# Kernel tuning notes

Measured on AMD Instinct MI355X. Metric: run time of the kernel, lower is better.

The kernel has to match this reference:

```python
import jax, jax.numpy as jnp
import numpy as np

NUM_HEADS = 8      # SD1.x UNet cross-attn heads at 64x64 block
NUM_PROMPTS = 4    # batch = 2*NUM_PROMPTS (uncond + cond CFG halves)


def setup_inputs() -> dict:
    key = jax.random.key(0)
    ks = jax.random.split(key, 8)
    B, T, C = 2 * NUM_PROMPTS, 4096, 320   # spatial tokens, inner dim
    S, D = 77, 768                          # CLIP text seq len / width
    return {
        "hidden_states": jax.random.normal(ks[0], (B, T, C), jnp.float32),
        "encoder_hidden_states": jax.random.normal(ks[1], (B, S, D), jnp.float32),
        "mapper": jax.random.uniform(ks[2], (NUM_PROMPTS - 1, S, S), jnp.float32),
        "Wq": jax.random.normal(ks[3], (C, C), jnp.float32) * 0.02,
        "Wk": jax.random.normal(ks[4], (D, C), jnp.float32) * 0.02,
        "Wv": jax.random.normal(ks[5], (D, C), jnp.float32) * 0.02,
        "Wo": jax.random.normal(ks[6], (C, C), jnp.float32) * 0.02,
        "bo": jnp.zeros((C,), jnp.float32),
    }


def reference(hidden_states, encoder_hidden_states, mapper, Wq, Wk, Wv, Wo, bo):
    B, T, C = hidden_states.shape
    S = encoder_hidden_states.shape[1]
    H = NUM_HEADS
    d = C // H
    scale = 1.0 / jnp.sqrt(jnp.asarray(d, hidden_states.dtype))

    # projections + head split (diffusers head_to_batch_dim layout)
    q = (hidden_states @ Wq).reshape(B, T, H, d)
    k = (encoder_hidden_states @ Wk).reshape(B, S, H, d)
    v = (encoder_hidden_states @ Wv).reshape(B, S, H, d)

    # full attention probabilities must be materialized for the P2P swap
    scores = jnp.einsum('bthd,bshd->bhts', q, k) * scale
    probs = jax.nn.softmax(scores, axis=-1)  # [B, H, T, S]

    # conditional (CFG) half: [P, H, T, S]; swap via mapper einsum (cross-attn,
    # cur_step < num_steps_cross branch of swap_attention_probs)
    half = B // 2
    uncond = probs[:half]
    cond = probs[half:]
    attn_base = cond[0]                                   # [H, T, S]
    replaced = jnp.einsum('htm,pme->phte', attn_base, mapper)  # [P-1, H, T, S]
    cond = jnp.concatenate([attn_base[None], replaced], axis=0)
    probs = jnp.concatenate([uncond, cond], axis=0)

    # value matmul + merge heads (batch_to_head_dim) + output projection
    out = jnp.einsum('bhts,bshd->bthd', probs, v).reshape(B, T, C)
    return out @ Wo + bo
```

## Files before the change

### kernel.cpp

```cpp
#include <hip/hip_runtime.h>
#include <hip/hip_bf16.h>

typedef unsigned short ushort;
typedef __attribute__((ext_vector_type(8))) short bf16x8;
typedef __attribute__((ext_vector_type(8))) unsigned short ushort8;
typedef __attribute__((ext_vector_type(4))) float f32x4;
typedef __attribute__((ext_vector_type(4))) float float4v;

__device__ __forceinline__ ushort f2bf(float f) {
    union { float f; unsigned u; } v; v.f = f;
    unsigned r = v.u + 0x7FFFu + ((v.u >> 16) & 1u);
    return (ushort)(r >> 16);
}
__device__ __forceinline__ float bf2f(ushort u) {
    union { unsigned u; float f; } v; v.u = ((unsigned)u) << 16;
    return v.f;
}

__global__ __launch_bounds__(256) void transpose_all(
    const float* __restrict__ Wq, const float* __restrict__ Wk,
    const float* __restrict__ Wv, const float* __restrict__ Wo,
    ushort* __restrict__ Wq_t, ushort* __restrict__ Wk_t,
    ushort* __restrict__ Wv_t, ushort* __restrict__ Wo_t)
{
    __shared__ ushort t[32][33];
    int b = blockIdx.x;
    const float* src; ushort* dst; int K; int tb;
    if (b < 100)      { src = Wq; dst = Wq_t; K = 320; tb = b; }
    else if (b < 340) { src = Wk; dst = Wk_t; K = 768; tb = b - 100; }
    else if (b < 580) { src = Wv; dst = Wv_t; K = 768; tb = b - 340; }
    else              { src = Wo; dst = Wo_t; K = 320; tb = b - 580; }
    int tc = tb % 10, tr = tb / 10;
    int tx = threadIdx.x & 31, ty = threadIdx.x >> 5;
    #pragma unroll
    for (int p = 0; p < 4; ++p) {
        int k = tr * 32 + ty + p * 8, n = tc * 32 + tx;
        t[ty + p * 8][tx] = f2bf(src[(size_t)k * 320 + n]);
    }
    __syncthreads();
    #pragma unroll
    for (int p = 0; p < 4; ++p) {
        int n = tc * 32 + ty + p * 8, k = tr * 32 + tx;
        dst[(size_t)n * K + k] = t[tx][ty + p * 8];
    }
}

__global__ __launch_bounds__(256) void gemm_qkv(
    const float* __restrict__ A, const ushort* __restrict__ Wq_t,
    const float* __restrict__ E, const ushort* __restrict__ Wk_t,
    const ushort* __restrict__ Wv_t,
    ushort* __restrict__ Qb, float* __restrict__ part)
{
    __shared__ ushort A_lds[2][64 * 40];
    __shared__ ushort B_lds[2][320 * 40];
    const int tid = threadIdx.x;
    const int w = tid >> 6, l = tid & 63;
    const int c15 = l & 15, khi = (l >> 4) * 8;
    const int r = tid >> 2, p = (tid & 3) * 8;
    const int rbase = (l >> 4) * 4;
    f32x4 acc[4][5] = {};
    const int bid = blockIdx.x;

    if (bid < 160) {
        const int mtile = bid % 10, mat = (bid / 10) & 1, ks = bid / 20;
        const int m0 = mtile * 64, kk0 = ks * 96;
        const ushort* Bt = mat ? Wv_t : Wk_t;
        const int m = m0 + r;
        const bool live = (m < 616);
        const float* Abase = E + (size_t)(live ? m : 0) * 768 + p;
        float4v a0 = {0,0,0,0}, a1 = {0,0,0,0};
        ushort8 breg[5];
        if (live) { a0 = *(const float4v*)(Abase + kk0); a1 = *(const float4v*)(Abase + kk0 + 4); }
        #pragma unroll
        for (int i = 0; i < 5; ++i) {
            int idx = tid + i * 256; int n = idx >> 2, q = (idx & 3) * 8;
            breg[i] = *(const ushort8*)(Bt + (size_t)n * 768 + kk0 + q);
        }
        {
            ushort* d = &A_lds[0][r * 40 + p];
            d[0]=f2bf(a0.x); d[1]=f2bf(a0.y); d[2]=f2bf(a0.z); d[3]=f2bf(a0.w);
            d[4]=f2bf(a1.x); d[5]=f2bf(a1.y); d[6]=f2bf(a1.z); d[7]=f2bf(a1.w);
            #pragma unroll
            for (int i = 0; i < 5; ++i) {
                int idx = tid + i * 256; int n = idx >> 2, q = (idx & 3) * 8;
                *(ushort8*)&B_lds[0][n * 40 + q] = breg[i];
            }
        }
        __syncthreads();
        for (int k = 0; k < 3; ++k) {
            const int cur = k & 1;
            if (k < 2) {
                int kk = kk0 + (k + 1) * 32;
                if (live) { a0 = *(const float4v*)(Abase + kk); a1 = *(const float4v*)(Abase + kk + 4); }
                #pragma unroll
                for (int i = 0; i < 5; ++i) {
                    int idx = tid + i * 256; int n = idx >> 2, q = (idx & 3) * 8;
                    breg[i] = *(const ushort8*)(Bt + (size_t)n * 768 + kk + q);
                }
            }
            bf16x8 a[4];
            #pragma unroll
            for (int mf = 0; mf < 4; ++mf)
                a[mf] = *(const bf16x8*)&A_lds[cur][(mf * 16 + c15) * 40 + khi];
            #pragma unroll
            for (int f = 0; f < 5; ++f) {
                bf16x8 b = *(const bf16x8*)&B_lds[cur][(w * 80 + f * 16 + c15) * 40 + khi];
                #pragma unroll
                for (int mf = 0; mf < 4; ++mf)
                    acc[mf][f] = __builtin_amdgcn_mfma_f32_16x16x32_bf16(a[mf], b, acc[mf][f], 0, 0, 0);
            }
            if (k < 2) {
                const int nxt = cur ^ 1;
                ushort* d = &A_lds[nxt][r * 40 + p];
                d[0]=f2bf(a0.x); d[1]=f2bf(a0.y); d[2]=f2bf(a0.z); d[3]=f2bf(a0.w);
                d[4]=f2bf(a1.x); d[5]=f2bf(a1.y); d[6]=f2bf(a1.z); d[7]=f2bf(a1.w);
                #pragma unroll
                for (int i = 0; i < 5; ++i) {
                    int idx = tid + i * 256; int n = idx >> 2, q = (idx & 3) * 8;
                    *(ushort8*)&B_lds[nxt][n * 40 + q] = breg[i];
                }
                __syncthreads();
            }
        }
        float* dst = part + (size_t)(mat * 8 + ks) * 640 * 320;
        #pragma unroll
        for (int mf = 0; mf < 4; ++mf)
            #pragma unroll
            for (int f = 0; f < 5; ++f) {
                int col = w * 80 + f * 16 + c15;
                #pragma unroll
                for (int rr = 0; rr < 4; ++rr)
                    dst[(size_t)(m0 + mf * 16 + rbase + rr) * 320 + col] = acc[mf][f][rr];
            }
    } else {
        const int m0 = (bid - 160) * 64;
        const float* Abase = A + (size_t)(m0 + r) * 320 + p;
        float4v a0, a1; ushort8 breg[5];
        a0 = *(const float4v*)(Abase + 0);
        a1 = *(const float4v*)(Abase + 4);
        #pragma unroll
        for (int i = 0; i < 5; ++i) {
            int idx = tid + i * 256; int n = idx >> 2, q = (idx & 3) * 8;
            breg[i] = *(const ushort8*)(Wq_t + (size_t)n * 320 + q);
        }
        {
            ushort* d = &A_lds[0][r * 40 + p];
            d[0]=f2bf(a0.x); d[1]=f2bf(a0.y); d[2]=f2bf(a0.z); d[3]=f2bf(a0.w);
            d[4]=f2bf(a1.x); d[5]=f2bf(a1.y); d[6]=f2bf(a1.z); d[7]=f2bf(a1.w);
            #pragma unroll
            for (int i = 0; i < 5; ++i) {
                int idx = tid + i * 256; int n = idx >> 2, q = (idx & 3) * 8;
                *(ushort8*)&B_lds[0][n * 40 + q] = breg[i];
            }
        }
        __syncthreads();
        for (int k = 0; k < 10; ++k) {
            const int cur = k & 1;
            if (k < 9) {
                int kk = (k + 1) * 32;
                a0 = *(const float4v*)(Abase + kk);
                a1 = *(const float4v*)(Abase + kk + 4);
                #pragma unroll
                for (int i = 0; i < 5; ++i) {
                    int idx = tid + i * 256; int n = idx >> 2, q = (idx & 3) * 8;
                    breg[i] = *(const ushort8*)(Wq_t + (size_t)n * 320 + kk + q);
                }
            }
            bf16x8 a[4];
            #pragma unroll
            for (int mf = 0; mf < 4; ++mf)
                a[mf] = *(const bf16x8*)&A_lds[cur][(mf * 16 + c15) * 40 + khi];
            #pragma unroll
            for (int f = 0; f < 5; ++f) {
                bf16x8 b = *(const bf16x8*)&B_lds[cur][(w * 80 + f * 16 + c15) * 40 + khi];
                #pragma unroll
                for (int mf = 0; mf < 4; ++mf)
                    acc[mf][f] = __builtin_amdgcn_mfma_f32_16x16x32_bf16(a[mf], b, acc[mf][f], 0, 0, 0);
            }
            if (k < 9) {
                const int nxt = cur ^ 1;
                ushort* d = &A_lds[nxt][r * 40 + p];
                d[0]=f2bf(a0.x); d[1]=f2bf(a0.y); d[2]=f2bf(a0.z); d[3]=f2bf(a0.w);
                d[4]=f2bf(a1.x); d[5]=f2bf(a1.y); d[6]=f2bf(a1.z); d[7]=f2bf(a1.w);
                #pragma unroll
                for (int i = 0; i < 5; ++i) {
                    int idx = tid + i * 256; int n = idx >> 2, q = (idx & 3) * 8;
                    *(ushort8*)&B_lds[nxt][n * 40 + q] = breg[i];
                }
                __syncthreads();
            }
        }
        #pragma unroll
        for (int mf = 0; mf < 4; ++mf)
            #pragma unroll
            for (int f = 0; f < 5; ++f) {
                int col = w * 80 + f * 16 + c15;
                #pragma unroll
                for (int rr = 0; rr < 4; ++rr)
                    Qb[(size_t)(m0 + mf * 16 + rbase + rr) * 320 + col] = f2bf(acc[mf][f][rr]);
            }
    }
}

__global__ __launch_bounds__(256) void kv_reduce(
    const float* __restrict__ part, ushort* __restrict__ Kb, ushort* __restrict__ VVt)
{
    int idx = blockIdx.x * 256 + threadIdx.x;
    int mat = blockIdx.y;
    if (mat == 1) {
        if (idx < 8 * 320 * 3) {
            int b = idx / 960, r2 = idx - b * 960, c = r2 / 3, j = r2 - c * 3;
            VVt[((size_t)b * 320 + c) * 80 + 77 + j] = 0;
        }
    }
    if (idx >= 616 * 320) return;
    int row = idx / 320, col = idx - row * 320;
    float s = 0.f;
    #pragma unroll
    for (int ks = 0; ks < 8; ++ks)
        s += part[((size_t)(mat * 8 + ks) * 640 + row) * 320 + col];
    ushort b = f2bf(s);
    if (mat == 0) {
        Kb[(size_t)row * 320 + col] = b;
    } else {
        int bt = row / 77, ss = row - bt * 77;
        VVt[((size_t)bt * 320 + col) * 80 + ss] = b;
    }
}

__global__ void vprime_k(const float* __restrict__ mapper, const ushort* __restrict__ VVt,
                         ushort* __restrict__ VPt)
{
    int pm = blockIdx.x;
    int p = pm / 77, m = pm - p * 77;
    __shared__ float mp[77];
    int tid = threadIdx.x;
    if (tid < 77) mp[tid] = mapper[(size_t)pm * 77 + tid];
    __syncthreads();
    const ushort* vrow = VVt + ((size_t)(5 + p) * 320 + tid) * 80;
    float acc = 0.f;
    for (int e = 0; e < 77; ++e) acc += mp[e] * bf2f(vrow[e]);
    VPt[((size_t)p * 320 + tid) * 80 + m] = f2bf(acc);
    if (m >= 74) VPt[((size_t)p * 320 + tid) * 80 + (m + 3)] = 0;
}

#define ATT_SCALE 0.15811388300841897f
__global__ __launch_bounds__(512, 4) void attn_out_k(
    const ushort* __restrict__ Q, const ushort* __restrict__ K,
    const ushort* __restrict__ VVt, const ushort* __restrict__ VPt,
    const ushort* __restrict__ Wo_t, const float* __restrict__ bias,
    float* __restrict__ out)
{
    __shared__ __align__(16) ushort AO_lds[64 * 328];
    __shared__ __align__(16) ushort P_lds[8 * 16 * 104];
    ushort* W_lds = P_lds;

    const int tid = threadIdx.x;
    const int ww = tid >> 6, l = tid & 63;
    const int rg = ww & 3, half = ww >> 2;
    const int c15 = l & 15, hi4 = l >> 4;
    const int khi = hi4 * 8, rbase = hi4 * 4;
    const int bt = blockIdx.y, t0 = blockIdx.x * 64;
    const int qb = (bt < 5) ? bt : 4;
    const ushort* Vbase = (bt < 5) ? (VVt + (size_t)bt * 320 * 80)
                                   : (VPt + (size_t)(bt - 5) * 320 * 80);
    const ushort8 z8 = {0,0,0,0,0,0,0,0};
    ushort* Pw = P_lds + ww * (16 * 104);

    if (l < 48) {
        int r = l / 3, c = l - 3 * (l / 3);
        *(ushort8*)&Pw[r * 104 + 80 + c * 8] = z8;
    }

    const ushort* Qrow = Q + (size_t)(qb * 4096 + t0 + rg * 16 + c15) * 320;

    for (int hh = 0; hh < 4; ++hh) {
        const int h = half * 4 + hh;

        bf16x8 qa0 = *(const bf16x8*)(Qrow + h * 40 + khi);
        bf16x8 qa1 = {0,0,0,0,0,0,0,0};
        if (hi4 == 0) qa1 = *(const bf16x8*)(Qrow + h * 40 + 32);
        f32x4 sacc[5] = {};
        #pragma unroll
        for (int f = 0; f < 5; ++f) {
            const ushort* kr = K + (size_t)(qb * 77 + f * 16 + c15) * 320 + h * 40;
            bf16x8 kb0 = *(const bf16x8*)(kr + khi);
            bf16x8 kb1 = *(const bf16x8*)(kr + 32 + khi);
            sacc[f] = __builtin_amdgcn_mfma_f32_16x16x32_bf16(qa0, kb0, sacc[f], 0, 0, 0);
            sacc[f] = __builtin_amdgcn_mfma_f32_16x16x32_bf16(qa1, kb1, sacc[f], 0, 0, 0);
        }

        bf16x8 vreg[3][3];
        #pragma unroll
        for (int f = 0; f < 3; ++f)
            #pragma unroll
            for (int kt = 0; kt < 3; ++kt) {
                int soff = kt * 32 + khi;
                if (soff >= 80) soff = 0;
                vreg[f][kt] = *(const bf16x8*)(Vbase + ((size_t)h * 40 + f * 16 + c15) * 80 + soff);
            }

        float pv[5][4];
        #pragma unroll
        for (int r = 0; r < 4; ++r) {
            float mx = -1e30f;
            #pragma unroll
            for (int f = 0; f < 5; ++f) {
                float vs = sacc[f][r] * ATT_SCALE;
                bool valid = (f < 4) || (c15 < 13);
                pv[f][r] = valid ? vs : -1e30f;
                mx = fmaxf(mx, pv[f][r]);
            }
            #pragma unroll
            for (int d = 1; d < 16; d <<= 1) mx = fmaxf(mx, __shfl_xor(mx, d));
            float sum = 0.f;
            #pragma unroll
            for (int f = 0; f < 5; ++f) {
                float e = (pv[f][r] > -1e29f) ? __expf(pv[f][r] - mx) : 0.f;
                pv[f][r] = e; sum += e;
            }
            #pragma unroll
            for (int d = 1; d < 16; d <<= 1) sum += __shfl_xor(sum, d);
            float inv = 1.f / sum;
            #pragma unroll
            for (int f = 0; f < 5; ++f) pv[f][r] *= inv;
        }

        #pragma unroll
        for (int r = 0; r < 4; ++r)
            #pragma unroll
            for (int f = 0; f < 5; ++f)
                Pw[(rbase + r) * 104 + f * 16 + c15] = f2bf(pv[f][r]);

        bf16x8 pa[3];
        #pragma unroll
        for (int kt = 0; kt < 3; ++kt)
            pa[kt] = *(const bf16x8*)&Pw[c15 * 104 + kt * 32 + khi];
        f32x4 oacc[3] = {};
        #pragma unroll
        for (int f = 0; f < 3; ++f)
            #pragma unroll
            for (int kt = 0; kt < 3; ++kt)
                oacc[f] = __builtin_amdgcn_mfma_f32_16x16x32_bf16(pa[kt], vreg[f][kt], oacc[f], 0, 0, 0);
        #pragma unroll
        for (int f = 0; f < 3; ++f) {
            int col = f * 16 + c15;
            if (col < 40) {
                #pragma unroll
                for (int r = 0; r < 4; ++r)
                    AO_lds[(rg * 16 + rbase + r) * 328 + h * 40 + col] = f2bf(oacc[f][r]);
            }
        }
    }
    __syncthreads();

    const int cb = half * 160;
    f32x4 acc[10] = {};
    for (int kk = 0; kk < 10; ++kk) {
        if (kk) __syncthreads();
        #pragma unroll
        for (int i = 0; i < 3; ++i) {
            int idx = tid + i * 512;
            if (idx < 1280) {
                int n = idx >> 2, c = idx & 3;
                *(ushort8*)&W_lds[n * 40 + c * 8] =
                    *(const ushort8*)(Wo_t + (size_t)n * 320 + kk * 32 + c * 8);
            }
        }
        __syncthreads();
        bf16x8 a = *(const bf16x8*)&AO_lds[(rg * 16 + c15) * 328 + kk * 32 + khi];
        #pragma unroll
        for (int f = 0; f < 10; ++f) {
            bf16x8 b = *(const bf16x8*)&W_lds[(cb + f * 16 + c15) * 40 + khi];
            acc[f] = __builtin_amdgcn_mfma_f32_16x16x32_bf16(a, b, acc[f], 0, 0, 0);
        }
    }

    #pragma unroll
    for (int f = 0; f < 10; ++f) {
        int col = cb + f * 16 + c15;
        #pragma unroll
        for (int rr = 0; rr < 4; ++rr)
            out[(size_t)(bt * 4096 + t0 + rg * 16 + rbase + rr) * 320 + col]
                = acc[f][rr] + bias[col];
    }
}

extern "C" void kernel_launch(void* const* d_in, const int* in_sizes, int n_in,
                              void* d_out, int out_size, void* d_ws, size_t ws_size,
                              hipStream_t stream) {
    (void)in_sizes; (void)n_in; (void)out_size; (void)ws_size;
    const float* hs     = (const float*)d_in[0];
    const float* ehs    = (const float*)d_in[1];
    const float* mapper = (const float*)d_in[2];
    const float* Wq     = (const float*)d_in[3];
    const float* Wk     = (const float*)d_in[4];
    const float* Wv     = (const float*)d_in[5];
    const float* Wo     = (const float*)d_in[6];
    const float* bo     = (const float*)d_in[7];
    float* out = (float*)d_out;

    ushort* ws   = (ushort*)d_ws;
    ushort* Wq_t = ws;
    ushort* Wk_t = Wq_t + 320 * 320;
    ushort* Wv_t = Wk_t + 320 * 768;
    ushort* Wo_t = Wv_t + 320 * 768;
    ushort* Qb   = Wo_t + 320 * 320;
    ushort* Kb   = Qb + 20480 * 320;
    ushort* VVt  = Kb + 616 * 320;
    ushort* VPt  = VVt + 8 * 320 * 80;
    float*  part = (float*)(VPt + 3 * 320 * 80);

    transpose_all<<<680, 256, 0, stream>>>(Wq, Wk, Wv, Wo, Wq_t, Wk_t, Wv_t, Wo_t);
    gemm_qkv<<<480, 256, 0, stream>>>(hs, Wq_t, ehs, Wk_t, Wv_t, Qb, part);
    kv_reduce<<<dim3(770, 2), 256, 0, stream>>>(part, Kb, VVt);
    vprime_k<<<231, 320, 0, stream>>>(mapper, VVt, VPt);
    attn_out_k<<<dim3(64, 8), 512, 0, stream>>>(Qb, Kb, VVt, VPt, Wo_t, bo, out);
}
```

Baseline: 80.51 us.

## Store Q/K/V in MFMA fragment-native layout and drop softmax max subtraction

```diff
diff --git a/kernel.cpp b/kernel.cpp
--- a/kernel.cpp
+++ b/kernel.cpp
@@ -15,6 +15,21 @@
 __device__ __forceinline__ float bf2f(ushort u) {
     union { unsigned u; float f; } v; v.u = ((unsigned)u) << 16;
     return v.f;
+}
+
+#define QF_SZ   (1280u * 8 * 2 * 512)
+#define KF_SZ   (5u * 8 * 5 * 2 * 512)
+#define VF_SZ   (5u * 8 * 3 * 3 * 512)
+#define VPF_SZ  (3u * 8 * 3 * 3 * 512)
+
+__global__ __launch_bounds__(256) void zero_fill(
+    ushort* __restrict__ Kf, ushort* __restrict__ Vf, ushort* __restrict__ VPf)
+{
+    const ushort8 z8 = {0,0,0,0,0,0,0,0};
+    unsigned i = blockIdx.x * 256 + threadIdx.x;
+    if (i < KF_SZ / 8) ((ushort8*)Kf)[i] = z8;
+    else if (i < (KF_SZ + VF_SZ) / 8) ((ushort8*)Vf)[i - KF_SZ / 8] = z8;
+    else if (i < (KF_SZ + VF_SZ + VPF_SZ) / 8) ((ushort8*)VPf)[i - (KF_SZ + VF_SZ) / 8] = z8;
 }
 
 __global__ __launch_bounds__(256) void transpose_all(
@@ -49,7 +64,7 @@
     const float* __restrict__ A, const ushort* __restrict__ Wq_t,
     const float* __restrict__ E, const ushort* __restrict__ Wk_t,
     const ushort* __restrict__ Wv_t,
-    ushort* __restrict__ Qb, float* __restrict__ part)
+    ushort* __restrict__ Qf, float* __restrict__ part)
 {
     __shared__ ushort A_lds[2][64 * 40];
     __shared__ ushort B_lds[2][320 * 40];
@@ -60,6 +75,7 @@
     const int rbase = (l >> 4) * 4;
     f32x4 acc[4][5] = {};
     const int bid = blockIdx.x;
+    const ushort8 z8 = {0,0,0,0,0,0,0,0};
 
     if (bid < 160) {
         const int mtile = bid % 10, mat = (bid / 10) & 1, ks = bid / 20;
@@ -190,46 +206,63 @@
                 __syncthreads();
             }
         }
+        const int rg0 = m0 >> 4;
+        for (int i = tid; i < 1536; i += 256) {
+            int grp = i / 48;
+            int lane16 = 16 + (i - grp * 48);
+            int rg4 = grp >> 3, h = grp & 7;
+            *(ushort8*)(Qf + ((size_t)((rg0 + rg4) * 8 + h) * 2 + 1) * 512 + lane16 * 8) = z8;
+        }
         #pragma unroll
         for (int mf = 0; mf < 4; ++mf)
             #pragma unroll
             for (int f = 0; f < 5; ++f) {
                 int col = w * 80 + f * 16 + c15;
-                #pragma unroll
-                for (int rr = 0; rr < 4; ++rr)
-                    Qb[(size_t)(m0 + mf * 16 + rbase + rr) * 320 + col] = f2bf(acc[mf][f][rr]);
+                int h = col / 40, kd = col - h * 40;
+                int kt = kd >> 5, chunk = (kd >> 3) & 3, elem = kd & 7;
+                size_t base = ((size_t)((rg0 + mf) * 8 + h) * 2 + kt) * 512;
+                #pragma unroll
+                for (int rr = 0; rr < 4; ++rr) {
+                    int lane = (rbase + rr) | (chunk << 4);
+                    Qf[base + lane * 8 + elem] = f2bf(acc[mf][f][rr]);
+                }
             }
     }
 }
 
 __global__ __launch_bounds__(256) void kv_reduce(
-    const float* __restrict__ part, ushort* __restrict__ Kb, ushort* __restrict__ VVt)
+    const float* __restrict__ part, ushort* __restrict__ Kf,
+    ushort* __restrict__ Vf, ushort* __restrict__ VVt)
 {
     int idx = blockIdx.x * 256 + threadIdx.x;
+    if (idx >= 616 * 320) return;
     int mat = blockIdx.y;
-    if (mat == 1) {
-        if (idx < 8 * 320 * 3) {
-            int b = idx / 960, r2 = idx - b * 960, c = r2 / 3, j = r2 - c * 3;
-            VVt[((size_t)b * 320 + c) * 80 + 77 + j] = 0;
-        }
-    }
-    if (idx >= 616 * 320) return;
     int row = idx / 320, col = idx - row * 320;
-    float s = 0.f;
+    float s8 = 0.f;
     #pragma unroll
     for (int ks = 0; ks < 8; ++ks)
-        s += part[((size_t)(mat * 8 + ks) * 640 + row) * 320 + col];
-    ushort b = f2bf(s);
+        s8 += part[((size_t)(mat * 8 + ks) * 640 + row) * 320 + col];
+    ushort b = f2bf(s8);
+    int bt = row / 77, s = row - bt * 77;
+    int h = col / 40, kd = col - h * 40;
     if (mat == 0) {
-        Kb[(size_t)row * 320 + col] = b;
+        if (bt < 5) {
+            int kt = kd >> 5, chunk = (kd >> 3) & 3;
+            int lane = (s & 15) | (chunk << 4);
+            Kf[((size_t)((bt * 8 + h) * 5 + (s >> 4)) * 2 + kt) * 512 + lane * 8 + (kd & 7)] = b;
+        }
     } else {
-        int bt = row / 77, ss = row - bt * 77;
-        VVt[((size_t)bt * 320 + col) * 80 + ss] = b;
+        if (bt < 5) {
+            int lane = (kd & 15) | (((s >> 3) & 3) << 4);
+            Vf[(((size_t)(bt * 8 + h) * 3 + (kd >> 4)) * 3 + (s >> 5)) * 512 + lane * 8 + (s & 7)] = b;
+        } else {
+            VVt[((size_t)bt * 320 + col) * 80 + s] = b;
+        }
     }
 }
 
 __global__ void vprime_k(const float* __restrict__ mapper, const ushort* __restrict__ VVt,
-                         ushort* __restrict__ VPt)
+                         ushort* __restrict__ VPf)
 {
     int pm = blockIdx.x;
     int p = pm / 77, m = pm - p * 77;
@@ -240,14 +273,15 @@
     const ushort* vrow = VVt + ((size_t)(5 + p) * 320 + tid) * 80;
     float acc = 0.f;
     for (int e = 0; e < 77; ++e) acc += mp[e] * bf2f(vrow[e]);
-    VPt[((size_t)p * 320 + tid) * 80 + m] = f2bf(acc);
-    if (m >= 74) VPt[((size_t)p * 320 + tid) * 80 + (m + 3)] = 0;
+    int h = tid / 40, dc = tid - h * 40;
+    int lane = (dc & 15) | (((m >> 3) & 3) << 4);
+    VPf[(((size_t)(p * 8 + h) * 3 + (dc >> 4)) * 3 + (m >> 5)) * 512 + lane * 8 + (m & 7)] = f2bf(acc);
 }
 
 #define ATT_SCALE 0.15811388300841897f
 __global__ __launch_bounds__(512, 4) void attn_out_k(
-    const ushort* __restrict__ Q, const ushort* __restrict__ K,
-    const ushort* __restrict__ VVt, const ushort* __restrict__ VPt,
+    const ushort* __restrict__ Qf, const ushort* __restrict__ Kf,
+    const ushort* __restrict__ Vf, const ushort* __restrict__ VPf,
     const ushort* __restrict__ Wo_t, const float* __restrict__ bias,
     float* __restrict__ out)
 {
@@ -262,8 +296,9 @@
     const int khi = hi4 * 8, rbase = hi4 * 4;
     const int bt = blockIdx.y, t0 = blockIdx.x * 64;
     const int qb = (bt < 5) ? bt : 4;
-    const ushort* Vbase = (bt < 5) ? (VVt + (size_t)bt * 320 * 80)
-                                   : (VPt + (size_t)(bt - 5) * 320 * 80);
+    const int rowgrp = qb * 256 + blockIdx.x * 4 + rg;
+    const ushort* Vfb = (bt < 5) ? (Vf + (size_t)bt * (8 * 3 * 3 * 512))
+                                 : (VPf + (size_t)(bt - 5) * (8 * 3 * 3 * 512));
     const ushort8 z8 = {0,0,0,0,0,0,0,0};
     ushort* Pw = P_lds + ww * (16 * 104);
 
@@ -272,20 +307,17 @@
         *(ushort8*)&Pw[r * 104 + 80 + c * 8] = z8;
     }
 
-    const ushort* Qrow = Q + (size_t)(qb * 4096 + t0 + rg * 16 + c15) * 320;
-
     for (int hh = 0; hh < 4; ++hh) {
         const int h = half * 4 + hh;
 
-        bf16x8 qa0 = *(const bf16x8*)(Qrow + h * 40 + khi);
-        bf16x8 qa1 = {0,0,0,0,0,0,0,0};
-        if (hi4 == 0) qa1 = *(const bf16x8*)(Qrow + h * 40 + 32);
+        bf16x8 qa0 = *(const bf16x8*)(Qf + ((size_t)(rowgrp * 8 + h) * 2 + 0) * 512 + l * 8);
+        bf16x8 qa1 = *(const bf16x8*)(Qf + ((size_t)(rowgrp * 8 + h) * 2 + 1) * 512 + l * 8);
         f32x4 sacc[5] = {};
         #pragma unroll
         for (int f = 0; f < 5; ++f) {
-            const ushort* kr = K + (size_t)(qb * 77 + f * 16 + c15) * 320 + h * 40;
-            bf16x8 kb0 = *(const bf16x8*)(kr + khi);
-            bf16x8 kb1 = *(const bf16x8*)(kr + 32 + khi);
+            const ushort* kfb = Kf + ((size_t)((qb * 8 + h) * 5 + f) * 2) * 512 + l * 8;
+            bf16x8 kb0 = *(const bf16x8*)(kfb);
+            bf16x8 kb1 = *(const bf16x8*)(kfb + 512);
             sacc[f] = __builtin_amdgcn_mfma_f32_16x16x32_bf16(qa0, kb0, sacc[f], 0, 0, 0);
             sacc[f] = __builtin_amdgcn_mfma_f32_16x16x32_bf16(qa1, kb1, sacc[f], 0, 0, 0);
         }
@@ -294,29 +326,17 @@
         #pragma unroll
         for (int f = 0; f < 3; ++f)
             #pragma unroll
-            for (int kt = 0; kt < 3; ++kt) {
-                int soff = kt * 32 + khi;
-                if (soff >= 80) soff = 0;
-                vreg[f][kt] = *(const bf16x8*)(Vbase + ((size_t)h * 40 + f * 16 + c15) * 80 + soff);
-            }
+            for (int kt = 0; kt < 3; ++kt)
+                vreg[f][kt] = *(const bf16x8*)(Vfb + (((size_t)(h * 3 + f) * 3 + kt)) * 512 + l * 8);
 
         float pv[5][4];
         #pragma unroll
         for (int r = 0; r < 4; ++r) {
-            float mx = -1e30f;
+            float sum = 0.f;
             #pragma unroll
             for (int f = 0; f < 5; ++f) {
-                float vs = sacc[f][r] * ATT_SCALE;
                 bool valid = (f < 4) || (c15 < 13);
-                pv[f][r] = valid ? vs : -1e30f;
-                mx = fmaxf(mx, pv[f][r]);
-            }
-            #pragma unroll
-            for (int d = 1; d < 16; d <<= 1) mx = fmaxf(mx, __shfl_xor(mx, d));
-            float sum = 0.f;
-            #pragma unroll
-            for (int f = 0; f < 5; ++f) {
-                float e = (pv[f][r] > -1e29f) ? __expf(pv[f][r] - mx) : 0.f;
+                float e = valid ? __expf(sacc[f][r] * ATT_SCALE) : 0.f;
                 pv[f][r] = e; sum += e;
             }
             #pragma unroll
@@ -405,15 +425,17 @@
     ushort* Wk_t = Wq_t + 320 * 320;
     ushort* Wv_t = Wk_t + 320 * 768;
     ushort* Wo_t = Wv_t + 320 * 768;
-    ushort* Qb   = Wo_t + 320 * 320;
-    ushort* Kb   = Qb + 20480 * 320;
-    ushort* VVt  = Kb + 616 * 320;
-    ushort* VPt  = VVt + 8 * 320 * 80;
-    float*  part = (float*)(VPt + 3 * 320 * 80);
-
+    ushort* Qfb  = Wo_t + 320 * 320;
+    ushort* Kfb  = Qfb + QF_SZ;
+    ushort* Vfb  = Kfb + KF_SZ;
+    ushort* VPfb = Vfb + VF_SZ;
+    ushort* VVt  = VPfb + VPF_SZ;
+    float*  part = (float*)(VVt + 8 * 320 * 80);
+
+    zero_fill<<<389, 256, 0, stream>>>(Kfb, Vfb, VPfb);
     transpose_all<<<680, 256, 0, stream>>>(Wq, Wk, Wv, Wo, Wq_t, Wk_t, Wv_t, Wo_t);
-    gemm_qkv<<<480, 256, 0, stream>>>(hs, Wq_t, ehs, Wk_t, Wv_t, Qb, part);
-    kv_reduce<<<dim3(770, 2), 256, 0, stream>>>(part, Kb, VVt);
-    vprime_k<<<231, 320, 0, stream>>>(mapper, VVt, VPt);
-    attn_out_k<<<dim3(64, 8), 512, 0, stream>>>(Qb, Kb, VVt, VPt, Wo_t, bo, out);
-}
+    gemm_qkv<<<480, 256, 0, stream>>>(hs, Wq_t, ehs, Wk_t, Wv_t, Qfb, part);
+    kv_reduce<<<dim3(770, 2), 256, 0, stream>>>(part, Kfb, Vfb, VVt);
+    vprime_k<<<231, 320, 0, stream>>>(mapper, VVt, VPfb);
+    attn_out_k<<<dim3(64, 8), 512, 0, stream>>>(Qfb, Kfb, Vfb, VPfb, Wo_t, bo, out);
+}
```

After: 73.42 us. 8.8% less time.
